# Performance work log

Hardware: AMD Instinct MI355X
Metric: run time of the kernel (lower is better)

The kernel has to match this reference:

```python
import jax, jax.numpy as jnp
import numpy as np

NX = 4096
NY = 4096
DX = 0.01
DY = 0.01
DT = 0.001
CX = 1.0
CY = 1.0
CXW = DT / DX / 2.0 * CX  # 0.05, x-direction stencil coefficient
CYW = DT / DY / 2.0 * CY  # 0.05, y-direction stencil coefficient
DIAG = 1.0                # A[1,1]
NLEVEL = int(np.log2(min(NX, NY))) + 1  # 13


def _smooth(x):
    # 3x3 cross-correlation with kernel A, valid padding (stride 1, no pad).
    # A[0,1]=CYW, A[2,1]=-CYW, A[1,0]=CXW, A[1,1]=1, A[1,2]=-CXW.
    return (CYW * x[:-2, 1:-1] - CYW * x[2:, 1:-1]
            + CXW * x[1:-1, :-2] + x[1:-1, 1:-1] - CXW * x[1:-1, 2:])


def _bc(u):
    # Replicate edges (not corners: corners stay exactly 0, as in the torch code).
    H, W = u.shape
    p = jnp.zeros((H + 2, W + 2), u.dtype)
    p = p.at[1:-1, 1:-1].set(u)
    p = p.at[0, 1:-1].set(u[0])
    p = p.at[-1, 1:-1].set(u[-1])
    p = p.at[1:-1, 0].set(u[:, 0])
    p = p.at[1:-1, -1].set(u[:, -1])
    return p


def _restrict(x):
    # 2x2 average pooling, stride 2 (conv weight = 0.25 everywhere).
    return 0.25 * (x[0::2, 0::2] + x[1::2, 0::2] + x[0::2, 1::2] + x[1::2, 1::2])


def _prolong(x):
    # Nearest-neighbor upsample by 2.
    return jnp.repeat(jnp.repeat(x, 2, axis=0), 2, axis=1)


def setup_inputs() -> dict:
    key = jax.random.key(0)
    u = jax.random.normal(key, (1, 1, NY, NX), dtype=jnp.float32)
    return {"u": u, "t": 4}


def reference(u, t):
    v = u[0, 0]  # (NY, NX)
    for _ in range(t):  # t outer F-cycle iterations (b = 0 source term)
        r = _smooth(_bc(v))  # residual on finest grid, (NY, NX)
        r_s = [r]
        for _i in range(1, NLEVEL - 3):
            r = _restrict(r)
            r_s.append(r)  # coarsest stored level is 8x8
        e = jnp.zeros((1, 1), v.dtype)
        for j in reversed(range(1, NLEVEL - 3)):
            # coarse-grid correction; broadcast of (small e) + r_s[j] matches torch
            e = e - _smooth(jnp.pad(e, 1)) / DIAG + r_s[j] / DIAG
            e = _prolong(e)
        v = v - e
        v = v - _smooth(_bc(v)) / DIAG
    return v[None, None]
```

## Files before the change

kernel.cpp:

```cpp
#include <hip/hip_runtime.h>
#include <cstddef>


constexpr float CW = 0.05f;

__device__ __forceinline__ float up_val(float Pc, float Pu, float Pd, float Pl,
                                        float Pr, float rv) {
  float sm = CW * Pu - CW * Pd + CW * Pl + Pc - CW * Pr;
  return (Pc - sm) + rv;
}

__global__ __launch_bounds__(256) void k_smooth_restrict(
    const float* __restrict__ v, float* __restrict__ r1) {
  const int n = 4096, h = 2048;
  int bj = blockIdx.x * blockDim.x + threadIdx.x;
  int bi = blockIdx.y * blockDim.y + threadIdx.y;
  int c0 = 4 * bj;
  int cl = max(c0 - 1, 0), cr = min(c0 + 4, n - 1);
  float a[6][6];
#pragma unroll
  for (int rr = 0; rr < 6; ++rr) {
    int R = min(max(4 * bi - 1 + rr, 0), n - 1);
    const float* row = v + (size_t)R * n;
    float4 m = *reinterpret_cast<const float4*>(row + c0);
    a[rr][0] = row[cl];
    a[rr][1] = m.x; a[rr][2] = m.y; a[rr][3] = m.z; a[rr][4] = m.w;
    a[rr][5] = row[cr];
  }
#pragma unroll
  for (int oi = 0; oi < 2; ++oi) {
    float2 o;
#pragma unroll
    for (int oj = 0; oj < 2; ++oj) {
      float s[2][2];
#pragma unroll
      for (int p = 0; p < 2; ++p)
#pragma unroll
        for (int q = 0; q < 2; ++q) {
          int P = 2 * oi + p, Q = 2 * oj + q;
          s[p][q] = CW * a[P][Q + 1] - CW * a[P + 2][Q + 1]
                  + CW * a[P + 1][Q] + a[P + 1][Q + 1] - CW * a[P + 1][Q + 2];
        }
      float val = 0.25f * (((s[0][0] + s[1][0]) + s[0][1]) + s[1][1]);
      (oj ? o.y : o.x) = val;
    }
    *reinterpret_cast<float2*>(r1 + (size_t)(2 * bi + oi) * h + 2 * bj) = o;
  }
}

__global__ __launch_bounds__(256) void k_restrict2(
    const float* __restrict__ x, float* __restrict__ y,
    float* __restrict__ z, int n) {
  int h = n >> 1, q = n >> 2;
  int j = blockIdx.x * blockDim.x + threadIdx.x;
  int i = blockIdx.y * blockDim.y + threadIdx.y;
  if (i >= q || 2 * j >= q) return;
  float xr[4][8];
#pragma unroll
  for (int rr = 0; rr < 4; ++rr) {
    const float* row = x + (size_t)(4 * i + rr) * n + 8 * j;
    float4 m0 = reinterpret_cast<const float4*>(row)[0];
    float4 m1 = reinterpret_cast<const float4*>(row)[1];
    xr[rr][0] = m0.x; xr[rr][1] = m0.y; xr[rr][2] = m0.z; xr[rr][3] = m0.w;
    xr[rr][4] = m1.x; xr[rr][5] = m1.y; xr[rr][6] = m1.z; xr[rr][7] = m1.w;
  }
  float yv[2][4];
#pragma unroll
  for (int a = 0; a < 2; ++a)
#pragma unroll
    for (int b = 0; b < 4; ++b)
      yv[a][b] = 0.25f * (((xr[2 * a][2 * b] + xr[2 * a + 1][2 * b])
                           + xr[2 * a][2 * b + 1]) + xr[2 * a + 1][2 * b + 1]);
#pragma unroll
  for (int a = 0; a < 2; ++a) {
    float4 o; o.x = yv[a][0]; o.y = yv[a][1]; o.z = yv[a][2]; o.w = yv[a][3];
    *reinterpret_cast<float4*>(y + (size_t)(2 * i + a) * h + 4 * j) = o;
  }
  float2 zo;
  zo.x = 0.25f * (((yv[0][0] + yv[1][0]) + yv[0][1]) + yv[1][1]);
  zo.y = 0.25f * (((yv[0][2] + yv[1][2]) + yv[0][3]) + yv[1][3]);
  *reinterpret_cast<float2*>(z + (size_t)i * q + 2 * j) = zo;
}

__global__ __launch_bounds__(256) void k_up(
    const float* __restrict__ Ep, const float* __restrict__ r,
    float* __restrict__ Eo, int n) {
  int s = n >> 1;
  int j = blockIdx.x * blockDim.x + threadIdx.x;
  int i = blockIdx.y * blockDim.y + threadIdx.y;
  if (i >= s || j >= (n >> 2)) return;
  const float* ec = Ep + (size_t)i * s + 2 * j;
  float epc0 = ec[0], epc1 = ec[1];
  float epl = (j > 0) ? ec[-1] : 0.0f;
  float epr = (2 * j + 2 < s) ? ec[2] : 0.0f;
  float epu0 = 0.0f, epu1 = 0.0f, epd0 = 0.0f, epd1 = 0.0f;
  if (i > 0)     { epu0 = ec[-s]; epu1 = ec[-s + 1]; }
  if (i < s - 1) { epd0 = ec[s];  epd1 = ec[s + 1]; }
  {
    float4 rv = *reinterpret_cast<const float4*>(r + (size_t)(2 * i) * n + 4 * j);
    float4 o;
    o.x = up_val(epc0, epu0, epc0, epl,  epc0, rv.x);
    o.y = up_val(epc0, epu0, epc0, epc0, epc1, rv.y);
    o.z = up_val(epc1, epu1, epc1, epc0, epc1, rv.z);
    o.w = up_val(epc1, epu1, epc1, epc1, epr,  rv.w);
    *reinterpret_cast<float4*>(Eo + (size_t)(2 * i) * n + 4 * j) = o;
  }
  {
    float4 rv = *reinterpret_cast<const float4*>(r + (size_t)(2 * i + 1) * n + 4 * j);
    float4 o;
    o.x = up_val(epc0, epc0, epd0, epl,  epc0, rv.x);
    o.y = up_val(epc0, epc0, epd0, epc0, epc1, rv.y);
    o.z = up_val(epc1, epc1, epd1, epc0, epc1, rv.z);
    o.w = up_val(epc1, epc1, epd1, epc1, epr,  rv.w);
    *reinterpret_cast<float4*>(Eo + (size_t)(2 * i + 1) * n + 4 * j) = o;
  }
}

__global__ void k_coarse(const float* __restrict__ r5, float* __restrict__ E5) {
  __shared__ float r6[64 * 64];
  __shared__ float r7[32 * 32];
  __shared__ float r8[16 * 16];
  __shared__ float r9[8 * 8];
  __shared__ float E8[16 * 16];
  __shared__ float E7[32 * 32];
  __shared__ float E6[64 * 64];
  int tid = threadIdx.x, nt = blockDim.x;

  auto up_lds = [&](const float* Ep, const float* rr, int i, int c, int nn) {
    int ss = nn >> 1;
    float Pc = Ep[(i >> 1) * ss + (c >> 1)];
    float Pu = (i > 0)      ? Ep[((i - 1) >> 1) * ss + (c >> 1)] : 0.0f;
    float Pd = (i < nn - 1) ? Ep[((i + 1) >> 1) * ss + (c >> 1)] : 0.0f;
    float Pl = (c > 0)      ? Ep[(i >> 1) * ss + ((c - 1) >> 1)] : 0.0f;
    float Pr = (c < nn - 1) ? Ep[(i >> 1) * ss + ((c + 1) >> 1)] : 0.0f;
    return up_val(Pc, Pu, Pd, Pl, Pr, rr[i * nn + c]);
  };

  for (int idx = tid; idx < 64 * 64; idx += nt) {
    int I = idx >> 6, J = idx & 63;
    float a = r5[(2 * I) * 128 + 2 * J],     b = r5[(2 * I + 1) * 128 + 2 * J];
    float c = r5[(2 * I) * 128 + 2 * J + 1], d = r5[(2 * I + 1) * 128 + 2 * J + 1];
    r6[idx] = 0.25f * (((a + b) + c) + d);
  }
  __syncthreads();
  for (int idx = tid; idx < 32 * 32; idx += nt) {
    int I = idx >> 5, J = idx & 31;
    float a = r6[(2 * I) * 64 + 2 * J],     b = r6[(2 * I + 1) * 64 + 2 * J];
    float c = r6[(2 * I) * 64 + 2 * J + 1], d = r6[(2 * I + 1) * 64 + 2 * J + 1];
    r7[idx] = 0.25f * (((a + b) + c) + d);
  }
  __syncthreads();
  for (int idx = tid; idx < 16 * 16; idx += nt) {
    int I = idx >> 4, J = idx & 15;
    float a = r7[(2 * I) * 32 + 2 * J],     b = r7[(2 * I + 1) * 32 + 2 * J];
    float c = r7[(2 * I) * 32 + 2 * J + 1], d = r7[(2 * I + 1) * 32 + 2 * J + 1];
    r8[idx] = 0.25f * (((a + b) + c) + d);
  }
  __syncthreads();
  for (int idx = tid; idx < 8 * 8; idx += nt) {
    int I = idx >> 3, J = idx & 7;
    float a = r8[(2 * I) * 16 + 2 * J],     b = r8[(2 * I + 1) * 16 + 2 * J];
    float c = r8[(2 * I) * 16 + 2 * J + 1], d = r8[(2 * I + 1) * 16 + 2 * J + 1];
    r9[idx] = 0.25f * (((a + b) + c) + d);
  }
  __syncthreads();
  for (int idx = tid; idx < 16 * 16; idx += nt)
    E8[idx] = up_lds(r9, r8, idx >> 4, idx & 15, 16);
  __syncthreads();
  for (int idx = tid; idx < 32 * 32; idx += nt)
    E7[idx] = up_lds(E8, r7, idx >> 5, idx & 31, 32);
  __syncthreads();
  for (int idx = tid; idx < 64 * 64; idx += nt)
    E6[idx] = up_lds(E7, r6, idx >> 6, idx & 63, 64);
  __syncthreads();
  for (int idx = tid; idx < 128 * 128; idx += nt)
    E5[idx] = up_lds(E6, r5, idx >> 7, idx & 127, 128);
}

__global__ __launch_bounds__(256) void k_final(
    const float* __restrict__ v, const float* __restrict__ E1,
    float* __restrict__ out) {
  const int n = 4096, h = 2048;
  int J = blockIdx.x * blockDim.x + threadIdx.x;
  int i = blockIdx.y * blockDim.y + threadIdx.y;
  int c0 = 4 * J;
  int cl = max(c0 - 1, 0), cr = min(c0 + 4, n - 1);
  int ecl = cl >> 1, ecr = cr >> 1;

  float e[3][4];
  int ers0 = max(2 * i - 1, 0) >> 1;
  int ers2 = min(2 * i + 2, n - 1) >> 1;
  const int ers[3] = {ers0, i, ers2};
#pragma unroll
  for (int t = 0; t < 3; ++t) {
    const float* erow = E1 + (size_t)ers[t] * h;
    e[t][0] = erow[ecl];
    e[t][1] = erow[2 * J];
    e[t][2] = erow[2 * J + 1];
    e[t][3] = erow[ecr];
  }

  float w[4][6];
  const int tmap[4] = {0, 1, 1, 2};
#pragma unroll
  for (int rr = 0; rr < 4; ++rr) {
    int R = min(max(2 * i - 1 + rr, 0), n - 1);
    int t = tmap[rr];
    const float* vrow = v + (size_t)R * n;
    float4 m = *reinterpret_cast<const float4*>(vrow + c0);
    w[rr][0] = vrow[cl] - e[t][0];
    w[rr][1] = m.x - e[t][1];
    w[rr][2] = m.y - e[t][1];
    w[rr][3] = m.z - e[t][2];
    w[rr][4] = m.w - e[t][2];
    w[rr][5] = vrow[cr] - e[t][3];
  }
#pragma unroll
  for (int a = 0; a < 2; ++a) {
    float4 o;
#pragma unroll
    for (int qq = 0; qq < 4; ++qq) {
      float ce = w[a + 1][qq + 1];
      float sm = CW * w[a][qq + 1] - CW * w[a + 2][qq + 1]
               + CW * w[a + 1][qq] + ce - CW * w[a + 1][qq + 2];
      (&o.x)[qq] = ce - sm;
    }
    *reinterpret_cast<float4*>(out + (size_t)(2 * i + a) * n + c0) = o;
  }
}

extern "C" void kernel_launch(void* const* d_in, const int* in_sizes, int n_in,
                              void* d_out, int out_size, void* d_ws, size_t ws_size,
                              hipStream_t stream) {
  (void)in_sizes; (void)n_in; (void)out_size;
  float* u = (float*)d_in[0];
  float* out = (float*)d_out;
  char* ws = (char*)d_ws;

  size_t off = 0;
  auto alloc = [&](size_t elems) {
    float* p = (float*)(ws + off);
    off += (elems * sizeof(float) + 255) & ~(size_t)255;
    return p;
  };
  float* r1 = alloc(2048 * 2048);
  float* r2 = alloc(1024 * 1024);
  float* r3 = alloc(512 * 512);
  float* r4 = alloc(256 * 256);
  float* r5 = alloc(128 * 128);
  float* E5 = alloc(128 * 128);
  float* E4 = alloc(256 * 256);
  float* E3 = alloc(512 * 512);
  float* E2 = alloc(1024 * 1024);
  float* E1 = alloc(2048 * 2048);
  size_t pool = off;
  const size_t VB = (size_t)4096 * 4096 * sizeof(float);
  bool big = ws_size >= pool + VB;
  float* vws = (float*)(ws + pool);

  dim3 b(64, 4);
  auto iterate = [&](const float* vin, float* vout) {
    k_smooth_restrict<<<dim3(16, 256), b, 0, stream>>>(vin, r1);
    k_restrict2<<<dim3(4, 128), b, 0, stream>>>(r1, r2, r3, 2048);
    k_restrict2<<<dim3(1, 32), b, 0, stream>>>(r3, r4, r5, 512);
    k_coarse<<<1, 1024, 0, stream>>>(r5, E5);
    k_up<<<dim3(1, 32), b, 0, stream>>>(E5, r4, E4, 256);
    k_up<<<dim3(2, 64), b, 0, stream>>>(E4, r3, E3, 512);
    k_up<<<dim3(4, 128), b, 0, stream>>>(E3, r2, E2, 1024);
    k_up<<<dim3(8, 256), b, 0, stream>>>(E2, r1, E1, 2048);
    k_final<<<dim3(16, 512), b, 0, stream>>>(vin, E1, vout);
  };

  if (big) {
    iterate(u, vws);
    iterate(vws, out);
    iterate(out, vws);
    iterate(vws, out);
  } else {
    iterate(u, out);
    iterate(out, u);
    iterate(u, out);
    iterate(out, u);
    hipMemcpyAsync(out, u, VB, hipMemcpyDeviceToDevice, stream);
  }
}
```

Before: 397.9 us.

## Fuse last prolongation, final smoothing and next-iteration residual restriction into one kernel

Replaces the finest k_up (building E1) and k_final with one tiled kernel. It computes the E1 tile in shared memory from E2 and r1, applies the correction and the post-smooth, writes v, and also computes the next iteration's smoothed-and-restricted residual from the new v. This drops the E1 round trip and the separate k_smooth_restrict pass in iterations 2-4, using double-buffered r1 storage. The cost is redundant halo computation, heavier shared-memory use per block (about 40 KB), and divisions and modulos in the index arithmetic.

```diff
diff --git a/kernel.cpp b/kernel.cpp
--- a/kernel.cpp
+++ b/kernel.cpp
@@ -177,55 +177,98 @@
     E5[idx] = up_lds(E6, r5, idx >> 7, idx & 127, 128);
 }
 
-__global__ __launch_bounds__(256) void k_final(
-    const float* __restrict__ v, const float* __restrict__ E1,
-    float* __restrict__ out) {
-  const int n = 4096, h = 2048;
-  int J = blockIdx.x * blockDim.x + threadIdx.x;
-  int i = blockIdx.y * blockDim.y + threadIdx.y;
-  int c0 = 4 * J;
-  int cl = max(c0 - 1, 0), cr = min(c0 + 4, n - 1);
-  int ecl = cl >> 1, ecr = cr >> 1;
-
-  float e[3][4];
-  int ers0 = max(2 * i - 1, 0) >> 1;
-  int ers2 = min(2 * i + 2, n - 1) >> 1;
-  const int ers[3] = {ers0, i, ers2};
-#pragma unroll
-  for (int t = 0; t < 3; ++t) {
-    const float* erow = E1 + (size_t)ers[t] * h;
-    e[t][0] = erow[ecl];
-    e[t][1] = erow[2 * J];
-    e[t][2] = erow[2 * J + 1];
-    e[t][3] = erow[ecr];
-  }
-
-  float w[4][6];
-  const int tmap[4] = {0, 1, 1, 2};
-#pragma unroll
-  for (int rr = 0; rr < 4; ++rr) {
-    int R = min(max(2 * i - 1 + rr, 0), n - 1);
-    int t = tmap[rr];
-    const float* vrow = v + (size_t)R * n;
-    float4 m = *reinterpret_cast<const float4*>(vrow + c0);
-    w[rr][0] = vrow[cl] - e[t][0];
-    w[rr][1] = m.x - e[t][1];
-    w[rr][2] = m.y - e[t][1];
-    w[rr][3] = m.z - e[t][2];
-    w[rr][4] = m.w - e[t][2];
-    w[rr][5] = vrow[cr] - e[t][3];
-  }
-#pragma unroll
-  for (int a = 0; a < 2; ++a) {
+template <bool WRITE_R1>
+__global__ __launch_bounds__(256) void k_fused(
+    const float* __restrict__ v, const float* __restrict__ E2,
+    const float* __restrict__ r1, float* __restrict__ vout,
+    float* __restrict__ r1o) {
+  const int n = 4096, h = 2048, s2 = 1024;
+  const int BI = 16, BJ = 256;
+  __shared__ float e1s[10][132];
+  __shared__ float wsh[20][264];
+  __shared__ float vps[18][264];
+  int tid = threadIdx.x;
+  int x0 = blockIdx.x * BJ;
+  int y0 = blockIdx.y * BI;
+  int eb_r = (y0 >> 1) - 1;
+  int eb_c = (x0 >> 1) - 1;
+
+  for (int idx = tid; idx < 10 * 130; idx += 256) {
+    int er = idx / 130, ec = idx % 130;
+    int gi = min(max(eb_r + er, 0), h - 1);
+    int gc = min(max(eb_c + ec, 0), h - 1);
+    float Pc = E2[(size_t)(gi >> 1) * s2 + (gc >> 1)];
+    float Pu = (gi > 0)     ? E2[(size_t)((gi - 1) >> 1) * s2 + (gc >> 1)] : 0.0f;
+    float Pd = (gi < h - 1) ? E2[(size_t)((gi + 1) >> 1) * s2 + (gc >> 1)] : 0.0f;
+    float Pl = (gc > 0)     ? E2[(size_t)(gi >> 1) * s2 + ((gc - 1) >> 1)] : 0.0f;
+    float Pr = (gc < h - 1) ? E2[(size_t)(gi >> 1) * s2 + ((gc + 1) >> 1)] : 0.0f;
+    e1s[er][ec] = up_val(Pc, Pu, Pd, Pl, Pr, r1[(size_t)gi * h + gc]);
+  }
+  __syncthreads();
+
+  for (int idx = tid; idx < 20 * 64; idx += 256) {
+    int wr = idx >> 6, f = idx & 63;
+    int Rc = min(max(y0 - 2 + wr, 0), n - 1);
+    int er = (Rc >> 1) - eb_r;
+    float4 m = *reinterpret_cast<const float4*>(v + (size_t)Rc * n + x0 + 4 * f);
+    float e0 = e1s[er][2 * f + 1], e1v = e1s[er][2 * f + 2];
+    wsh[wr][2 + 4 * f]     = m.x - e0;
+    wsh[wr][2 + 4 * f + 1] = m.y - e0;
+    wsh[wr][2 + 4 * f + 2] = m.z - e1v;
+    wsh[wr][2 + 4 * f + 3] = m.w - e1v;
+  }
+  for (int idx = tid; idx < 20 * 4; idx += 256) {
+    int wr = idx >> 2, k = idx & 3;
+    int wc = (k < 2) ? k : 256 + k;
+    int Rc = min(max(y0 - 2 + wr, 0), n - 1);
+    int Cc = min(max(x0 - 2 + wc, 0), n - 1);
+    int er = (Rc >> 1) - eb_r;
+    int ec = (Cc >> 1) - eb_c;
+    wsh[wr][wc] = v[(size_t)Rc * n + Cc] - e1s[er][ec];
+  }
+  __syncthreads();
+
+  for (int idx = tid; idx < 18 * 258; idx += 256) {
+    int pr = idx / 258, pc = idx % 258;
+    float wc = wsh[pr + 1][pc + 1];
+    float sm = CW * wsh[pr][pc + 1] - CW * wsh[pr + 2][pc + 1]
+             + CW * wsh[pr + 1][pc] + wc - CW * wsh[pr + 1][pc + 2];
+    vps[pr][pc] = wc - sm;
+  }
+  __syncthreads();
+
+  for (int idx = tid; idx < 16 * 64; idx += 256) {
+    int rr = idx >> 6, f = idx & 63;
     float4 o;
-#pragma unroll
-    for (int qq = 0; qq < 4; ++qq) {
-      float ce = w[a + 1][qq + 1];
-      float sm = CW * w[a][qq + 1] - CW * w[a + 2][qq + 1]
-               + CW * w[a + 1][qq] + ce - CW * w[a + 1][qq + 2];
-      (&o.x)[qq] = ce - sm;
+    o.x = vps[rr + 1][4 * f + 1];
+    o.y = vps[rr + 1][4 * f + 2];
+    o.z = vps[rr + 1][4 * f + 3];
+    o.w = vps[rr + 1][4 * f + 4];
+    *reinterpret_cast<float4*>(vout + (size_t)(y0 + rr) * n + x0 + 4 * f) = o;
+  }
+
+  if constexpr (WRITE_R1) {
+    for (int idx = tid; idx < 8 * 128; idx += 256) {
+      int a = idx >> 7, b = idx & 127;
+      int gi = (y0 >> 1) + a, gj = (x0 >> 1) + b;
+      float sacc[2][2];
+#pragma unroll
+      for (int p = 0; p < 2; ++p)
+#pragma unroll
+        for (int q = 0; q < 2; ++q) {
+          int R = 2 * gi + p, C = 2 * gj + q;
+          int Ru = max(R - 1, 0), Rd = min(R + 1, n - 1);
+          int Cl = max(C - 1, 0), Cr = min(C + 1, n - 1);
+          float ce = vps[R - y0 + 1][C - x0 + 1];
+          sacc[p][q] = CW * vps[Ru - y0 + 1][C - x0 + 1]
+                     - CW * vps[Rd - y0 + 1][C - x0 + 1]
+                     + CW * vps[R - y0 + 1][Cl - x0 + 1]
+                     + ce
+                     - CW * vps[R - y0 + 1][Cr - x0 + 1];
+        }
+      r1o[(size_t)gi * h + gj] =
+          0.25f * (((sacc[0][0] + sacc[1][0]) + sacc[0][1]) + sacc[1][1]);
     }
-    *reinterpret_cast<float4*>(out + (size_t)(2 * i + a) * n + c0) = o;
   }
 }
 
@@ -243,7 +286,8 @@
     off += (elems * sizeof(float) + 255) & ~(size_t)255;
     return p;
   };
-  float* r1 = alloc(2048 * 2048);
+  float* r1a = alloc(2048 * 2048);
+  float* r1b = alloc(2048 * 2048);
   float* r2 = alloc(1024 * 1024);
   float* r3 = alloc(512 * 512);
   float* r4 = alloc(256 * 256);
@@ -252,35 +296,41 @@
   float* E4 = alloc(256 * 256);
   float* E3 = alloc(512 * 512);
   float* E2 = alloc(1024 * 1024);
-  float* E1 = alloc(2048 * 2048);
   size_t pool = off;
   const size_t VB = (size_t)4096 * 4096 * sizeof(float);
   bool big = ws_size >= pool + VB;
   float* vws = (float*)(ws + pool);
 
   dim3 b(64, 4);
-  auto iterate = [&](const float* vin, float* vout) {
-    k_smooth_restrict<<<dim3(16, 256), b, 0, stream>>>(vin, r1);
+  auto pyramid = [&](const float* r1) {
     k_restrict2<<<dim3(4, 128), b, 0, stream>>>(r1, r2, r3, 2048);
     k_restrict2<<<dim3(1, 32), b, 0, stream>>>(r3, r4, r5, 512);
     k_coarse<<<1, 1024, 0, stream>>>(r5, E5);
     k_up<<<dim3(1, 32), b, 0, stream>>>(E5, r4, E4, 256);
     k_up<<<dim3(2, 64), b, 0, stream>>>(E4, r3, E3, 512);
     k_up<<<dim3(4, 128), b, 0, stream>>>(E3, r2, E2, 1024);
-    k_up<<<dim3(8, 256), b, 0, stream>>>(E2, r1, E1, 2048);
-    k_final<<<dim3(16, 512), b, 0, stream>>>(vin, E1, vout);
   };
-
+  dim3 fg(16, 256);
+
+  k_smooth_restrict<<<dim3(16, 256), b, 0, stream>>>(u, r1a);
   if (big) {
-    iterate(u, vws);
-    iterate(vws, out);
-    iterate(out, vws);
-    iterate(vws, out);
+    pyramid(r1a);
+    k_fused<true><<<fg, 256, 0, stream>>>(u, E2, r1a, vws, r1b);
+    pyramid(r1b);
+    k_fused<true><<<fg, 256, 0, stream>>>(vws, E2, r1b, out, r1a);
+    pyramid(r1a);
+    k_fused<true><<<fg, 256, 0, stream>>>(out, E2, r1a, vws, r1b);
+    pyramid(r1b);
+    k_fused<false><<<fg, 256, 0, stream>>>(vws, E2, r1b, out, nullptr);
   } else {
-    iterate(u, out);
-    iterate(out, u);
-    iterate(u, out);
-    iterate(out, u);
+    pyramid(r1a);
+    k_fused<true><<<fg, 256, 0, stream>>>(u, E2, r1a, out, r1b);
+    pyramid(r1b);
+    k_fused<true><<<fg, 256, 0, stream>>>(out, E2, r1b, u, r1a);
+    pyramid(r1a);
+    k_fused<true><<<fg, 256, 0, stream>>>(u, E2, r1a, out, r1b);
+    pyramid(r1b);
+    k_fused<false><<<fg, 256, 0, stream>>>(out, E2, r1b, u, nullptr);
     hipMemcpyAsync(out, u, VB, hipMemcpyDeviceToDevice, stream);
   }
 }
```

Measured after the change: 516.4 us. +29.8%, slower.

## Fuse restriction pyramid, coarse solve and prolongation into one persistent kernel with grid barriers

Applied to the files above, without the earlier changes.

Replaces the seven launches per iteration (two restrict kernels, the single-block coarse solve and four prolongation kernels) with one persistent 128-block kernel. Stages are separated by atomic-counter grid barriers, and a counter reset kernel runs once at the start. Every block recomputes the coarse levels 6-9 in LDS and produces only its own two rows of E4, so the serial single-block coarse stage disappears. This removes launch gaps and small-grid tail latency, but the big prolongation stages now run on only 128 blocks of 256 threads, which may underuse the GPU's bandwidth, and correctness relies on all 128 blocks being co-resident.

```diff
diff --git a/kernel.cpp b/kernel.cpp
--- a/kernel.cpp
+++ b/kernel.cpp
@@ -3,11 +3,30 @@
 
 
 constexpr float CW = 0.05f;
+#define NBLK 128u
 
 __device__ __forceinline__ float up_val(float Pc, float Pu, float Pd, float Pl,
                                         float Pr, float rv) {
   float sm = CW * Pu - CW * Pd + CW * Pl + Pc - CW * Pr;
   return (Pc - sm) + rv;
+}
+
+__device__ __forceinline__ void grid_barrier(unsigned int* cnt, unsigned int target) {
+  __syncthreads();
+  __threadfence();
+  if (threadIdx.x == 0) {
+    __hip_atomic_fetch_add(cnt, 1u, __ATOMIC_ACQ_REL, __HIP_MEMORY_SCOPE_AGENT);
+    while (__hip_atomic_load(cnt, __ATOMIC_RELAXED, __HIP_MEMORY_SCOPE_AGENT) < target) {
+      __builtin_amdgcn_s_sleep(1);
+    }
+  }
+  __syncthreads();
+  __threadfence();
+}
+
+__global__ void k_zero(unsigned int* p, int n) {
+  int i = blockIdx.x * blockDim.x + threadIdx.x;
+  if (i < n) p[i] = 0u;
 }
 
 __global__ __launch_bounds__(256) void k_smooth_restrict(
@@ -48,47 +67,11 @@
   }
 }
 
-__global__ __launch_bounds__(256) void k_restrict2(
-    const float* __restrict__ x, float* __restrict__ y,
-    float* __restrict__ z, int n) {
-  int h = n >> 1, q = n >> 2;
-  int j = blockIdx.x * blockDim.x + threadIdx.x;
-  int i = blockIdx.y * blockDim.y + threadIdx.y;
-  if (i >= q || 2 * j >= q) return;
-  float xr[4][8];
-#pragma unroll
-  for (int rr = 0; rr < 4; ++rr) {
-    const float* row = x + (size_t)(4 * i + rr) * n + 8 * j;
-    float4 m0 = reinterpret_cast<const float4*>(row)[0];
-    float4 m1 = reinterpret_cast<const float4*>(row)[1];
-    xr[rr][0] = m0.x; xr[rr][1] = m0.y; xr[rr][2] = m0.z; xr[rr][3] = m0.w;
-    xr[rr][4] = m1.x; xr[rr][5] = m1.y; xr[rr][6] = m1.z; xr[rr][7] = m1.w;
-  }
-  float yv[2][4];
-#pragma unroll
-  for (int a = 0; a < 2; ++a)
-#pragma unroll
-    for (int b = 0; b < 4; ++b)
-      yv[a][b] = 0.25f * (((xr[2 * a][2 * b] + xr[2 * a + 1][2 * b])
-                           + xr[2 * a][2 * b + 1]) + xr[2 * a + 1][2 * b + 1]);
-#pragma unroll
-  for (int a = 0; a < 2; ++a) {
-    float4 o; o.x = yv[a][0]; o.y = yv[a][1]; o.z = yv[a][2]; o.w = yv[a][3];
-    *reinterpret_cast<float4*>(y + (size_t)(2 * i + a) * h + 4 * j) = o;
-  }
-  float2 zo;
-  zo.x = 0.25f * (((yv[0][0] + yv[1][0]) + yv[0][1]) + yv[1][1]);
-  zo.y = 0.25f * (((yv[0][2] + yv[1][2]) + yv[0][3]) + yv[1][3]);
-  *reinterpret_cast<float2*>(z + (size_t)i * q + 2 * j) = zo;
-}
-
-__global__ __launch_bounds__(256) void k_up(
-    const float* __restrict__ Ep, const float* __restrict__ r,
-    float* __restrict__ Eo, int n) {
+__device__ __forceinline__ void up_tile24(const float* __restrict__ Ep,
+                                          const float* __restrict__ r,
+                                          float* __restrict__ Eo,
+                                          int n, int i, int j) {
   int s = n >> 1;
-  int j = blockIdx.x * blockDim.x + threadIdx.x;
-  int i = blockIdx.y * blockDim.y + threadIdx.y;
-  if (i >= s || j >= (n >> 2)) return;
   const float* ec = Ep + (size_t)i * s + 2 * j;
   float epc0 = ec[0], epc1 = ec[1];
   float epl = (j > 0) ? ec[-1] : 0.0f;
@@ -116,65 +99,162 @@
   }
 }
 
-__global__ void k_coarse(const float* __restrict__ r5, float* __restrict__ E5) {
-  __shared__ float r6[64 * 64];
-  __shared__ float r7[32 * 32];
-  __shared__ float r8[16 * 16];
-  __shared__ float r9[8 * 8];
-  __shared__ float E8[16 * 16];
-  __shared__ float E7[32 * 32];
-  __shared__ float E6[64 * 64];
-  int tid = threadIdx.x, nt = blockDim.x;
-
-  auto up_lds = [&](const float* Ep, const float* rr, int i, int c, int nn) {
-    int ss = nn >> 1;
-    float Pc = Ep[(i >> 1) * ss + (c >> 1)];
-    float Pu = (i > 0)      ? Ep[((i - 1) >> 1) * ss + (c >> 1)] : 0.0f;
-    float Pd = (i < nn - 1) ? Ep[((i + 1) >> 1) * ss + (c >> 1)] : 0.0f;
-    float Pl = (c > 0)      ? Ep[(i >> 1) * ss + ((c - 1) >> 1)] : 0.0f;
-    float Pr = (c < nn - 1) ? Ep[(i >> 1) * ss + ((c + 1) >> 1)] : 0.0f;
-    return up_val(Pc, Pu, Pd, Pl, Pr, rr[i * nn + c]);
-  };
-
-  for (int idx = tid; idx < 64 * 64; idx += nt) {
-    int I = idx >> 6, J = idx & 63;
-    float a = r5[(2 * I) * 128 + 2 * J],     b = r5[(2 * I + 1) * 128 + 2 * J];
-    float c = r5[(2 * I) * 128 + 2 * J + 1], d = r5[(2 * I + 1) * 128 + 2 * J + 1];
-    r6[idx] = 0.25f * (((a + b) + c) + d);
-  }
-  __syncthreads();
-  for (int idx = tid; idx < 32 * 32; idx += nt) {
-    int I = idx >> 5, J = idx & 31;
-    float a = r6[(2 * I) * 64 + 2 * J],     b = r6[(2 * I + 1) * 64 + 2 * J];
-    float c = r6[(2 * I) * 64 + 2 * J + 1], d = r6[(2 * I + 1) * 64 + 2 * J + 1];
-    r7[idx] = 0.25f * (((a + b) + c) + d);
-  }
-  __syncthreads();
-  for (int idx = tid; idx < 16 * 16; idx += nt) {
-    int I = idx >> 4, J = idx & 15;
-    float a = r7[(2 * I) * 32 + 2 * J],     b = r7[(2 * I + 1) * 32 + 2 * J];
-    float c = r7[(2 * I) * 32 + 2 * J + 1], d = r7[(2 * I + 1) * 32 + 2 * J + 1];
-    r8[idx] = 0.25f * (((a + b) + c) + d);
-  }
-  __syncthreads();
-  for (int idx = tid; idx < 8 * 8; idx += nt) {
-    int I = idx >> 3, J = idx & 7;
-    float a = r8[(2 * I) * 16 + 2 * J],     b = r8[(2 * I + 1) * 16 + 2 * J];
-    float c = r8[(2 * I) * 16 + 2 * J + 1], d = r8[(2 * I + 1) * 16 + 2 * J + 1];
-    r9[idx] = 0.25f * (((a + b) + c) + d);
-  }
-  __syncthreads();
-  for (int idx = tid; idx < 16 * 16; idx += nt)
-    E8[idx] = up_lds(r9, r8, idx >> 4, idx & 15, 16);
-  __syncthreads();
-  for (int idx = tid; idx < 32 * 32; idx += nt)
-    E7[idx] = up_lds(E8, r7, idx >> 5, idx & 31, 32);
-  __syncthreads();
-  for (int idx = tid; idx < 64 * 64; idx += nt)
-    E6[idx] = up_lds(E7, r6, idx >> 6, idx & 63, 64);
-  __syncthreads();
-  for (int idx = tid; idx < 128 * 128; idx += nt)
-    E5[idx] = up_lds(E6, r5, idx >> 7, idx & 127, 128);
+__global__ __launch_bounds__(256, 1) void k_pyramid(
+    const float* __restrict__ r1, float* __restrict__ r2,
+    float* __restrict__ r3, float* __restrict__ r4, float* __restrict__ r5,
+    float* __restrict__ E4, float* __restrict__ E3, float* __restrict__ E2,
+    float* __restrict__ E1, unsigned int* __restrict__ bars) {
+  __shared__ float r5s[128 * 128];
+  __shared__ float r6s[64 * 64];
+  __shared__ float r7s[32 * 32];
+  __shared__ float r8s[16 * 16];
+  __shared__ float r9s[8 * 8];
+  __shared__ float E8s[16 * 16];
+  __shared__ float E7s[32 * 32];
+  __shared__ float E6s[64 * 64];
+  __shared__ float e5r[3][128];
+  int tid = threadIdx.x;
+  int bid = blockIdx.x;
+  int g = bid * 256 + tid;
+
+  if (g < 16384) {
+    int i5 = g >> 7, j5 = g & 127;
+    const float* src = r1 + (size_t)(i5 << 4) * 2048 + (j5 << 4);
+    float rr2[8][8];
+#pragma unroll
+    for (int a = 0; a < 8; ++a) {
+      float ta[16], tb[16];
+      const float* ra = src + (size_t)(2 * a) * 2048;
+      const float* rb = ra + 2048;
+#pragma unroll
+      for (int q = 0; q < 4; ++q) {
+        *reinterpret_cast<float4*>(ta + 4 * q) = reinterpret_cast<const float4*>(ra)[q];
+        *reinterpret_cast<float4*>(tb + 4 * q) = reinterpret_cast<const float4*>(rb)[q];
+      }
+#pragma unroll
+      for (int b = 0; b < 8; ++b)
+        rr2[a][b] = 0.25f * (((ta[2 * b] + tb[2 * b]) + ta[2 * b + 1]) + tb[2 * b + 1]);
+      float* dst = r2 + (size_t)((i5 << 3) + a) * 1024 + (j5 << 3);
+      float4 o0, o1;
+      o0.x = rr2[a][0]; o0.y = rr2[a][1]; o0.z = rr2[a][2]; o0.w = rr2[a][3];
+      o1.x = rr2[a][4]; o1.y = rr2[a][5]; o1.z = rr2[a][6]; o1.w = rr2[a][7];
+      reinterpret_cast<float4*>(dst)[0] = o0;
+      reinterpret_cast<float4*>(dst)[1] = o1;
+    }
+    float rr3[4][4];
+#pragma unroll
+    for (int a = 0; a < 4; ++a) {
+#pragma unroll
+      for (int b = 0; b < 4; ++b)
+        rr3[a][b] = 0.25f * (((rr2[2 * a][2 * b] + rr2[2 * a + 1][2 * b])
+                              + rr2[2 * a][2 * b + 1]) + rr2[2 * a + 1][2 * b + 1]);
+      float4 o;
+      o.x = rr3[a][0]; o.y = rr3[a][1]; o.z = rr3[a][2]; o.w = rr3[a][3];
+      *reinterpret_cast<float4*>(r3 + (size_t)((i5 << 2) + a) * 512 + (j5 << 2)) = o;
+    }
+    float rr4[2][2];
+#pragma unroll
+    for (int a = 0; a < 2; ++a) {
+#pragma unroll
+      for (int b = 0; b < 2; ++b)
+        rr4[a][b] = 0.25f * (((rr3[2 * a][2 * b] + rr3[2 * a + 1][2 * b])
+                              + rr3[2 * a][2 * b + 1]) + rr3[2 * a + 1][2 * b + 1]);
+      float2 o;
+      o.x = rr4[a][0]; o.y = rr4[a][1];
+      *reinterpret_cast<float2*>(r4 + (size_t)((i5 << 1) + a) * 256 + (j5 << 1)) = o;
+    }
+    r5[(size_t)i5 * 128 + j5] =
+        0.25f * (((rr4[0][0] + rr4[1][0]) + rr4[0][1]) + rr4[1][1]);
+  }
+  grid_barrier(bars + 0, NBLK);
+
+  {
+    auto up_lds = [&](const float* Ep, const float* rr, int i, int c, int nn) {
+      int ss = nn >> 1;
+      float Pc = Ep[(i >> 1) * ss + (c >> 1)];
+      float Pu = (i > 0)      ? Ep[((i - 1) >> 1) * ss + (c >> 1)] : 0.0f;
+      float Pd = (i < nn - 1) ? Ep[((i + 1) >> 1) * ss + (c >> 1)] : 0.0f;
+      float Pl = (c > 0)      ? Ep[(i >> 1) * ss + ((c - 1) >> 1)] : 0.0f;
+      float Pr = (c < nn - 1) ? Ep[(i >> 1) * ss + ((c + 1) >> 1)] : 0.0f;
+      return up_val(Pc, Pu, Pd, Pl, Pr, rr[i * nn + c]);
+    };
+    for (int idx = tid; idx < 4096; idx += 256)
+      reinterpret_cast<float4*>(r5s)[idx] = reinterpret_cast<const float4*>(r5)[idx];
+    __syncthreads();
+    for (int idx = tid; idx < 64 * 64; idx += 256) {
+      int I = idx >> 6, J = idx & 63;
+      float a = r5s[(2 * I) * 128 + 2 * J],     b = r5s[(2 * I + 1) * 128 + 2 * J];
+      float c = r5s[(2 * I) * 128 + 2 * J + 1], d = r5s[(2 * I + 1) * 128 + 2 * J + 1];
+      r6s[idx] = 0.25f * (((a + b) + c) + d);
+    }
+    __syncthreads();
+    for (int idx = tid; idx < 32 * 32; idx += 256) {
+      int I = idx >> 5, J = idx & 31;
+      float a = r6s[(2 * I) * 64 + 2 * J],     b = r6s[(2 * I + 1) * 64 + 2 * J];
+      float c = r6s[(2 * I) * 64 + 2 * J + 1], d = r6s[(2 * I + 1) * 64 + 2 * J + 1];
+      r7s[idx] = 0.25f * (((a + b) + c) + d);
+    }
+    __syncthreads();
+    for (int idx = tid; idx < 16 * 16; idx += 256) {
+      int I = idx >> 4, J = idx & 15;
+      float a = r7s[(2 * I) * 32 + 2 * J],     b = r7s[(2 * I + 1) * 32 + 2 * J];
+      float c = r7s[(2 * I) * 32 + 2 * J + 1], d = r7s[(2 * I + 1) * 32 + 2 * J + 1];
+      r8s[idx] = 0.25f * (((a + b) + c) + d);
+    }
+    __syncthreads();
+    for (int idx = tid; idx < 8 * 8; idx += 256) {
+      int I = idx >> 3, J = idx & 7;
+      float a = r8s[(2 * I) * 16 + 2 * J],     b = r8s[(2 * I + 1) * 16 + 2 * J];
+      float c = r8s[(2 * I) * 16 + 2 * J + 1], d = r8s[(2 * I + 1) * 16 + 2 * J + 1];
+      r9s[idx] = 0.25f * (((a + b) + c) + d);
+    }
+    __syncthreads();
+    for (int idx = tid; idx < 16 * 16; idx += 256)
+      E8s[idx] = up_lds(r9s, r8s, idx >> 4, idx & 15, 16);
+    __syncthreads();
+    for (int idx = tid; idx < 32 * 32; idx += 256)
+      E7s[idx] = up_lds(E8s, r7s, idx >> 5, idx & 31, 32);
+    __syncthreads();
+    for (int idx = tid; idx < 64 * 64; idx += 256)
+      E6s[idx] = up_lds(E7s, r6s, idx >> 6, idx & 63, 64);
+    __syncthreads();
+    for (int idx = tid; idx < 3 * 128; idx += 256) {
+      int rr = idx >> 7, c = idx & 127;
+      int i = min(max(bid - 1 + rr, 0), 127);
+      e5r[rr][c] = up_lds(E6s, r5s, i, c, 128);
+    }
+    __syncthreads();
+    for (int idx = tid; idx < 512; idx += 256) {
+      int gi = 2 * bid + (idx >> 8);
+      int gc = idx & 255;
+      float Pc = e5r[1][gc >> 1];
+      float Pu = (gi > 0)   ? e5r[((gi - 1) >> 1) - bid + 1][gc >> 1] : 0.0f;
+      float Pd = (gi < 255) ? e5r[((gi + 1) >> 1) - bid + 1][gc >> 1] : 0.0f;
+      float Pl = (gc > 0)   ? e5r[1][(gc - 1) >> 1] : 0.0f;
+      float Pr = (gc < 255) ? e5r[1][(gc + 1) >> 1] : 0.0f;
+      E4[(size_t)gi * 256 + gc] = up_val(Pc, Pu, Pd, Pl, Pr, r4[(size_t)gi * 256 + gc]);
+    }
+  }
+  grid_barrier(bars + 1, NBLK);
+
+  {
+    int i = g >> 7, j = g & 127;
+    up_tile24(E4, r3, E3, 512, i, j);
+  }
+  grid_barrier(bars + 2, NBLK);
+
+#pragma unroll
+  for (int t = 0; t < 4; ++t) {
+    int tile = g + t * 32768;
+    up_tile24(E3, r2, E2, 1024, tile >> 8, tile & 255);
+  }
+  grid_barrier(bars + 3, NBLK);
+
+#pragma unroll
+  for (int t = 0; t < 16; ++t) {
+    int tile = g + t * 32768;
+    up_tile24(E2, r1, E1, 2048, tile >> 9, tile & 511);
+  }
 }
 
 __global__ __launch_bounds__(256) void k_final(
@@ -248,39 +328,35 @@
   float* r3 = alloc(512 * 512);
   float* r4 = alloc(256 * 256);
   float* r5 = alloc(128 * 128);
-  float* E5 = alloc(128 * 128);
   float* E4 = alloc(256 * 256);
   float* E3 = alloc(512 * 512);
   float* E2 = alloc(1024 * 1024);
   float* E1 = alloc(2048 * 2048);
+  unsigned int* bars = (unsigned int*)alloc(64);
   size_t pool = off;
   const size_t VB = (size_t)4096 * 4096 * sizeof(float);
   bool big = ws_size >= pool + VB;
   float* vws = (float*)(ws + pool);
 
   dim3 b(64, 4);
-  auto iterate = [&](const float* vin, float* vout) {
+  auto iterate = [&](const float* vin, float* vout, int it) {
     k_smooth_restrict<<<dim3(16, 256), b, 0, stream>>>(vin, r1);
-    k_restrict2<<<dim3(4, 128), b, 0, stream>>>(r1, r2, r3, 2048);
-    k_restrict2<<<dim3(1, 32), b, 0, stream>>>(r3, r4, r5, 512);
-    k_coarse<<<1, 1024, 0, stream>>>(r5, E5);
-    k_up<<<dim3(1, 32), b, 0, stream>>>(E5, r4, E4, 256);
-    k_up<<<dim3(2, 64), b, 0, stream>>>(E4, r3, E3, 512);
-    k_up<<<dim3(4, 128), b, 0, stream>>>(E3, r2, E2, 1024);
-    k_up<<<dim3(8, 256), b, 0, stream>>>(E2, r1, E1, 2048);
+    k_pyramid<<<NBLK, 256, 0, stream>>>(r1, r2, r3, r4, r5, E4, E3, E2, E1,
+                                        bars + 4 * it);
     k_final<<<dim3(16, 512), b, 0, stream>>>(vin, E1, vout);
   };
 
+  k_zero<<<1, 64, 0, stream>>>(bars, 16);
   if (big) {
-    iterate(u, vws);
-    iterate(vws, out);
-    iterate(out, vws);
-    iterate(vws, out);
+    iterate(u, vws, 0);
+    iterate(vws, out, 1);
+    iterate(out, vws, 2);
+    iterate(vws, out, 3);
   } else {
-    iterate(u, out);
-    iterate(out, u);
-    iterate(u, out);
-    iterate(out, u);
+    iterate(u, out, 0);
+    iterate(out, u, 1);
+    iterate(u, out, 2);
+    iterate(out, u, 3);
     hipMemcpyAsync(out, u, VB, hipMemcpyDeviceToDevice, stream);
   }
 }
```

Measured after the change: 808.5 us. +103.2%, slower.

## Fuse restriction chain and coarse/upsample levels into fewer kernels

Applied to the files above, without the earlier changes.

Merges the fine smooth-restrict and all restriction levels down to 128x128 into one tiled kernel that keeps intermediates in shared memory. The coarse solve is extended to produce E4 directly, with the block count raised from 1 to 16; each block recomputes the full coarse pyramid redundantly. Two upsample levels (E3 and E2) are fused with E3 held in LDS. This cuts the launch count per iteration from 9 to 5 and removes some intermediate global round trips, at the cost of redundant coarse work and lower occupancy in the chain kernel.

```diff
diff --git a/kernel.cpp b/kernel.cpp
--- a/kernel.cpp
+++ b/kernel.cpp
@@ -10,76 +10,228 @@
   return (Pc - sm) + rv;
 }
 
-__global__ __launch_bounds__(256) void k_smooth_restrict(
-    const float* __restrict__ v, float* __restrict__ r1) {
+__global__ __launch_bounds__(256) void k_sr_chain(
+    const float* __restrict__ v, float* __restrict__ r1,
+    float* __restrict__ r2, float* __restrict__ r3,
+    float* __restrict__ r4, float* __restrict__ r5) {
   const int n = 4096, h = 2048;
-  int bj = blockIdx.x * blockDim.x + threadIdx.x;
-  int bi = blockIdx.y * blockDim.y + threadIdx.y;
-  int c0 = 4 * bj;
-  int cl = max(c0 - 1, 0), cr = min(c0 + 4, n - 1);
-  float a[6][6];
-#pragma unroll
-  for (int rr = 0; rr < 6; ++rr) {
-    int R = min(max(4 * bi - 1 + rr, 0), n - 1);
-    const float* row = v + (size_t)R * n;
-    float4 m = *reinterpret_cast<const float4*>(row + c0);
-    a[rr][0] = row[cl];
-    a[rr][1] = m.x; a[rr][2] = m.y; a[rr][3] = m.z; a[rr][4] = m.w;
-    a[rr][5] = row[cr];
-  }
-#pragma unroll
-  for (int oi = 0; oi < 2; ++oi) {
-    float2 o;
-#pragma unroll
-    for (int oj = 0; oj < 2; ++oj) {
-      float s[2][2];
-#pragma unroll
-      for (int p = 0; p < 2; ++p)
-#pragma unroll
-        for (int q = 0; q < 2; ++q) {
-          int P = 2 * oi + p, Q = 2 * oj + q;
-          s[p][q] = CW * a[P][Q + 1] - CW * a[P + 2][Q + 1]
-                  + CW * a[P + 1][Q] + a[P + 1][Q + 1] - CW * a[P + 1][Q + 2];
-        }
-      float val = 0.25f * (((s[0][0] + s[1][0]) + s[0][1]) + s[1][1]);
-      (oj ? o.y : o.x) = val;
-    }
-    *reinterpret_cast<float2*>(r1 + (size_t)(2 * bi + oi) * h + 2 * bj) = o;
-  }
-}
-
-__global__ __launch_bounds__(256) void k_restrict2(
-    const float* __restrict__ x, float* __restrict__ y,
-    float* __restrict__ z, int n) {
-  int h = n >> 1, q = n >> 2;
-  int j = blockIdx.x * blockDim.x + threadIdx.x;
-  int i = blockIdx.y * blockDim.y + threadIdx.y;
-  if (i >= q || 2 * j >= q) return;
-  float xr[4][8];
-#pragma unroll
-  for (int rr = 0; rr < 4; ++rr) {
-    const float* row = x + (size_t)(4 * i + rr) * n + 8 * j;
-    float4 m0 = reinterpret_cast<const float4*>(row)[0];
-    float4 m1 = reinterpret_cast<const float4*>(row)[1];
-    xr[rr][0] = m0.x; xr[rr][1] = m0.y; xr[rr][2] = m0.z; xr[rr][3] = m0.w;
-    xr[rr][4] = m1.x; xr[rr][5] = m1.y; xr[rr][6] = m1.z; xr[rr][7] = m1.w;
-  }
-  float yv[2][4];
-#pragma unroll
-  for (int a = 0; a < 2; ++a)
-#pragma unroll
-    for (int b = 0; b < 4; ++b)
-      yv[a][b] = 0.25f * (((xr[2 * a][2 * b] + xr[2 * a + 1][2 * b])
-                           + xr[2 * a][2 * b + 1]) + xr[2 * a + 1][2 * b + 1]);
-#pragma unroll
-  for (int a = 0; a < 2; ++a) {
-    float4 o; o.x = yv[a][0]; o.y = yv[a][1]; o.z = yv[a][2]; o.w = yv[a][3];
-    *reinterpret_cast<float4*>(y + (size_t)(2 * i + a) * h + 4 * j) = o;
-  }
-  float2 zo;
-  zo.x = 0.25f * (((yv[0][0] + yv[1][0]) + yv[0][1]) + yv[1][1]);
-  zo.y = 0.25f * (((yv[0][2] + yv[1][2]) + yv[0][3]) + yv[1][3]);
-  *reinterpret_cast<float2*>(z + (size_t)i * q + 2 * j) = zo;
+  __shared__ float r1s[64][65];
+  __shared__ float r2s[32][33];
+  __shared__ float r3s[16][17];
+  __shared__ float r4s[8][9];
+  int tid = threadIdx.x;
+  int bx = blockIdx.x, by = blockIdx.y;
+  int ty0 = by * 64, tx0 = bx * 64;
+
+#pragma unroll
+  for (int k = 0; k < 4; ++k) {
+    int u = tid + 256 * k;
+    int uy = u >> 5, ux = u & 31;
+    int bi = (ty0 >> 1) + uy;
+    int bj = (tx0 >> 1) + ux;
+    int c0 = 4 * bj;
+    int cl = max(c0 - 1, 0), cr = min(c0 + 4, n - 1);
+    float a[6][6];
+#pragma unroll
+    for (int rr = 0; rr < 6; ++rr) {
+      int R = min(max(4 * bi - 1 + rr, 0), n - 1);
+      const float* row = v + (size_t)R * n;
+      float4 m = *reinterpret_cast<const float4*>(row + c0);
+      a[rr][0] = row[cl];
+      a[rr][1] = m.x; a[rr][2] = m.y; a[rr][3] = m.z; a[rr][4] = m.w;
+      a[rr][5] = row[cr];
+    }
+#pragma unroll
+    for (int oi = 0; oi < 2; ++oi) {
+      float2 o;
+#pragma unroll
+      for (int oj = 0; oj < 2; ++oj) {
+        float s[2][2];
+#pragma unroll
+        for (int p = 0; p < 2; ++p)
+#pragma unroll
+          for (int q = 0; q < 2; ++q) {
+            int P = 2 * oi + p, Q = 2 * oj + q;
+            s[p][q] = CW * a[P][Q + 1] - CW * a[P + 2][Q + 1]
+                    + CW * a[P + 1][Q] + a[P + 1][Q + 1] - CW * a[P + 1][Q + 2];
+          }
+        float val = 0.25f * (((s[0][0] + s[1][0]) + s[0][1]) + s[1][1]);
+        (oj ? o.y : o.x) = val;
+        r1s[2 * uy + oi][2 * ux + oj] = val;
+      }
+      *reinterpret_cast<float2*>(r1 + (size_t)(2 * bi + oi) * h + 2 * bj) = o;
+    }
+  }
+  __syncthreads();
+
+#pragma unroll
+  for (int k = 0; k < 4; ++k) {
+    int idx = tid + 256 * k;
+    int I = idx >> 5, J = idx & 31;
+    float val = 0.25f * (((r1s[2 * I][2 * J] + r1s[2 * I + 1][2 * J])
+                          + r1s[2 * I][2 * J + 1]) + r1s[2 * I + 1][2 * J + 1]);
+    r2s[I][J] = val;
+    r2[(size_t)(32 * by + I) * 1024 + 32 * bx + J] = val;
+  }
+  __syncthreads();
+
+  {
+    int I = tid >> 4, J = tid & 15;
+    float val = 0.25f * (((r2s[2 * I][2 * J] + r2s[2 * I + 1][2 * J])
+                          + r2s[2 * I][2 * J + 1]) + r2s[2 * I + 1][2 * J + 1]);
+    r3s[I][J] = val;
+    r3[(size_t)(16 * by + I) * 512 + 16 * bx + J] = val;
+  }
+  __syncthreads();
+
+  if (tid < 64) {
+    int I = tid >> 3, J = tid & 7;
+    float val = 0.25f * (((r3s[2 * I][2 * J] + r3s[2 * I + 1][2 * J])
+                          + r3s[2 * I][2 * J + 1]) + r3s[2 * I + 1][2 * J + 1]);
+    r4s[I][J] = val;
+    r4[(size_t)(8 * by + I) * 256 + 8 * bx + J] = val;
+  }
+  __syncthreads();
+
+  if (tid < 16) {
+    int I = tid >> 2, J = tid & 3;
+    float val = 0.25f * (((r4s[2 * I][2 * J] + r4s[2 * I + 1][2 * J])
+                          + r4s[2 * I][2 * J + 1]) + r4s[2 * I + 1][2 * J + 1]);
+    r5[(size_t)(4 * by + I) * 128 + 4 * bx + J] = val;
+  }
+}
+
+__global__ __launch_bounds__(1024, 1) void k_coarse_ext(
+    const float* __restrict__ r5, const float* __restrict__ r4,
+    float* __restrict__ E4) {
+  __shared__ float r5s[128 * 128];
+  __shared__ float r6s[64 * 64];
+  __shared__ float r7s[32 * 32];
+  __shared__ float r8s[16 * 16];
+  __shared__ float r9s[8 * 8];
+  __shared__ float E8s[16 * 16];
+  __shared__ float E7s[32 * 32];
+  __shared__ float E6s[64 * 64];
+  __shared__ float e5r[10][128];
+  int tid = threadIdx.x;
+  int bid = blockIdx.x;
+
+  auto up_lds = [&](const float* Ep, const float* rr, int i, int c, int nn) {
+    int ss = nn >> 1;
+    float Pc = Ep[(i >> 1) * ss + (c >> 1)];
+    float Pu = (i > 0)      ? Ep[((i - 1) >> 1) * ss + (c >> 1)] : 0.0f;
+    float Pd = (i < nn - 1) ? Ep[((i + 1) >> 1) * ss + (c >> 1)] : 0.0f;
+    float Pl = (c > 0)      ? Ep[(i >> 1) * ss + ((c - 1) >> 1)] : 0.0f;
+    float Pr = (c < nn - 1) ? Ep[(i >> 1) * ss + ((c + 1) >> 1)] : 0.0f;
+    return up_val(Pc, Pu, Pd, Pl, Pr, rr[i * nn + c]);
+  };
+
+  for (int idx = tid; idx < 4096; idx += 1024)
+    reinterpret_cast<float4*>(r5s)[idx] = reinterpret_cast<const float4*>(r5)[idx];
+  __syncthreads();
+  for (int idx = tid; idx < 64 * 64; idx += 1024) {
+    int I = idx >> 6, J = idx & 63;
+    float a = r5s[(2 * I) * 128 + 2 * J],     b = r5s[(2 * I + 1) * 128 + 2 * J];
+    float c = r5s[(2 * I) * 128 + 2 * J + 1], d = r5s[(2 * I + 1) * 128 + 2 * J + 1];
+    r6s[idx] = 0.25f * (((a + b) + c) + d);
+  }
+  __syncthreads();
+  if (tid < 32 * 32) {
+    int I = tid >> 5, J = tid & 31;
+    float a = r6s[(2 * I) * 64 + 2 * J],     b = r6s[(2 * I + 1) * 64 + 2 * J];
+    float c = r6s[(2 * I) * 64 + 2 * J + 1], d = r6s[(2 * I + 1) * 64 + 2 * J + 1];
+    r7s[tid] = 0.25f * (((a + b) + c) + d);
+  }
+  __syncthreads();
+  if (tid < 16 * 16) {
+    int I = tid >> 4, J = tid & 15;
+    float a = r7s[(2 * I) * 32 + 2 * J],     b = r7s[(2 * I + 1) * 32 + 2 * J];
+    float c = r7s[(2 * I) * 32 + 2 * J + 1], d = r7s[(2 * I + 1) * 32 + 2 * J + 1];
+    r8s[tid] = 0.25f * (((a + b) + c) + d);
+  }
+  __syncthreads();
+  if (tid < 8 * 8) {
+    int I = tid >> 3, J = tid & 7;
+    float a = r8s[(2 * I) * 16 + 2 * J],     b = r8s[(2 * I + 1) * 16 + 2 * J];
+    float c = r8s[(2 * I) * 16 + 2 * J + 1], d = r8s[(2 * I + 1) * 16 + 2 * J + 1];
+    r9s[tid] = 0.25f * (((a + b) + c) + d);
+  }
+  __syncthreads();
+  if (tid < 16 * 16)
+    E8s[tid] = up_lds(r9s, r8s, tid >> 4, tid & 15, 16);
+  __syncthreads();
+  if (tid < 32 * 32)
+    E7s[tid] = up_lds(E8s, r7s, tid >> 5, tid & 31, 32);
+  __syncthreads();
+  for (int idx = tid; idx < 64 * 64; idx += 1024)
+    E6s[idx] = up_lds(E7s, r6s, idx >> 6, idx & 63, 64);
+  __syncthreads();
+  for (int idx = tid; idx < 10 * 128; idx += 1024) {
+    int t = idx >> 7, c = idx & 127;
+    int i = min(max(8 * bid - 1 + t, 0), 127);
+    e5r[t][c] = up_lds(E6s, r5s, i, c, 128);
+  }
+  __syncthreads();
+  for (int idx = tid; idx < 16 * 256; idx += 1024) {
+    int gi = 16 * bid + (idx >> 8);
+    int gc = idx & 255;
+    float Pc = e5r[(gi >> 1) - 8 * bid + 1][gc >> 1];
+    float Pu = (gi > 0)   ? e5r[((gi - 1) >> 1) - 8 * bid + 1][gc >> 1] : 0.0f;
+    float Pd = (gi < 255) ? e5r[((gi + 1) >> 1) - 8 * bid + 1][gc >> 1] : 0.0f;
+    float Pl = (gc > 0)   ? e5r[(gi >> 1) - 8 * bid + 1][(gc - 1) >> 1] : 0.0f;
+    float Pr = (gc < 255) ? e5r[(gi >> 1) - 8 * bid + 1][(gc + 1) >> 1] : 0.0f;
+    E4[(size_t)gi * 256 + gc] = up_val(Pc, Pu, Pd, Pl, Pr, r4[(size_t)gi * 256 + gc]);
+  }
+}
+
+__global__ __launch_bounds__(256) void k_up_e3e2(
+    const float* __restrict__ E4, const float* __restrict__ r3,
+    const float* __restrict__ r2, float* __restrict__ E2) {
+  __shared__ float e3s[34][35];
+  int tid = threadIdx.x;
+  int bx = blockIdx.x, by = blockIdx.y;
+  int br0 = 32 * by - 1, bc0 = 32 * bx - 1;
+
+  for (int idx = tid; idx < 34 * 34; idx += 256) {
+    int er = idx / 34, ec = idx % 34;
+    int gr = br0 + er, gc = bc0 + ec;
+    float val = 0.0f;
+    if (gr >= 0 && gr < 512 && gc >= 0 && gc < 512) {
+      float Pc = E4[(size_t)(gr >> 1) * 256 + (gc >> 1)];
+      float Pu = (gr > 0)   ? E4[(size_t)((gr - 1) >> 1) * 256 + (gc >> 1)] : 0.0f;
+      float Pd = (gr < 511) ? E4[(size_t)((gr + 1) >> 1) * 256 + (gc >> 1)] : 0.0f;
+      float Pl = (gc > 0)   ? E4[(size_t)(gr >> 1) * 256 + ((gc - 1) >> 1)] : 0.0f;
+      float Pr = (gc < 511) ? E4[(size_t)(gr >> 1) * 256 + ((gc + 1) >> 1)] : 0.0f;
+      val = up_val(Pc, Pu, Pd, Pl, Pr, r3[(size_t)gr * 512 + gc]);
+    }
+    e3s[er][ec] = val;
+  }
+  __syncthreads();
+
+#pragma unroll
+  for (int k = 0; k < 4; ++k) {
+    int u = tid + 256 * k;
+    int rr = u >> 4, f = u & 15;
+    int gR = 64 * by + rr;
+    int gC = 64 * bx + 4 * f;
+    int rc = (gR >> 1) - br0;
+    int ru = ((gR - 1) >> 1) - br0;
+    int rd = ((gR + 1) >> 1) - br0;
+    float4 rv = *reinterpret_cast<const float4*>(r2 + (size_t)gR * 1024 + gC);
+    float4 o;
+#pragma unroll
+    for (int q = 0; q < 4; ++q) {
+      int c = gC + q;
+      int lc = (c >> 1) - bc0;
+      float Pc = e3s[rc][lc];
+      float Pu = (gR > 0)    ? e3s[ru][lc] : 0.0f;
+      float Pd = (gR < 1023) ? e3s[rd][lc] : 0.0f;
+      float Pl = (c > 0)     ? e3s[rc][((c - 1) >> 1) - bc0] : 0.0f;
+      float Pr = (c < 1023)  ? e3s[rc][((c + 1) >> 1) - bc0] : 0.0f;
+      (&o.x)[q] = up_val(Pc, Pu, Pd, Pl, Pr, (&rv.x)[q]);
+    }
+    *reinterpret_cast<float4*>(E2 + (size_t)gR * 1024 + gC) = o;
+  }
 }
 
 __global__ __launch_bounds__(256) void k_up(
@@ -116,67 +268,6 @@
   }
 }
 
-__global__ void k_coarse(const float* __restrict__ r5, float* __restrict__ E5) {
-  __shared__ float r6[64 * 64];
-  __shared__ float r7[32 * 32];
-  __shared__ float r8[16 * 16];
-  __shared__ float r9[8 * 8];
-  __shared__ float E8[16 * 16];
-  __shared__ float E7[32 * 32];
-  __shared__ float E6[64 * 64];
-  int tid = threadIdx.x, nt = blockDim.x;
-
-  auto up_lds = [&](const float* Ep, const float* rr, int i, int c, int nn) {
-    int ss = nn >> 1;
-    float Pc = Ep[(i >> 1) * ss + (c >> 1)];
-    float Pu = (i > 0)      ? Ep[((i - 1) >> 1) * ss + (c >> 1)] : 0.0f;
-    float Pd = (i < nn - 1) ? Ep[((i + 1) >> 1) * ss + (c >> 1)] : 0.0f;
-    float Pl = (c > 0)      ? Ep[(i >> 1) * ss + ((c - 1) >> 1)] : 0.0f;
-    float Pr = (c < nn - 1) ? Ep[(i >> 1) * ss + ((c + 1) >> 1)] : 0.0f;
-    return up_val(Pc, Pu, Pd, Pl, Pr, rr[i * nn + c]);
-  };
-
-  for (int idx = tid; idx < 64 * 64; idx += nt) {
-    int I = idx >> 6, J = idx & 63;
-    float a = r5[(2 * I) * 128 + 2 * J],     b = r5[(2 * I + 1) * 128 + 2 * J];
-    float c = r5[(2 * I) * 128 + 2 * J + 1], d = r5[(2 * I + 1) * 128 + 2 * J + 1];
-    r6[idx] = 0.25f * (((a + b) + c) + d);
-  }
-  __syncthreads();
-  for (int idx = tid; idx < 32 * 32; idx += nt) {
-    int I = idx >> 5, J = idx & 31;
-    float a = r6[(2 * I) * 64 + 2 * J],     b = r6[(2 * I + 1) * 64 + 2 * J];
-    float c = r6[(2 * I) * 64 + 2 * J + 1], d = r6[(2 * I + 1) * 64 + 2 * J + 1];
-    r7[idx] = 0.25f * (((a + b) + c) + d);
-  }
-  __syncthreads();
-  for (int idx = tid; idx < 16 * 16; idx += nt) {
-    int I = idx >> 4, J = idx & 15;
-    float a = r7[(2 * I) * 32 + 2 * J],     b = r7[(2 * I + 1) * 32 + 2 * J];
-    float c = r7[(2 * I) * 32 + 2 * J + 1], d = r7[(2 * I + 1) * 32 + 2 * J + 1];
-    r8[idx] = 0.25f * (((a + b) + c) + d);
-  }
-  __syncthreads();
-  for (int idx = tid; idx < 8 * 8; idx += nt) {
-    int I = idx >> 3, J = idx & 7;
-    float a = r8[(2 * I) * 16 + 2 * J],     b = r8[(2 * I + 1) * 16 + 2 * J];
-    float c = r8[(2 * I) * 16 + 2 * J + 1], d = r8[(2 * I + 1) * 16 + 2 * J + 1];
-    r9[idx] = 0.25f * (((a + b) + c) + d);
-  }
-  __syncthreads();
-  for (int idx = tid; idx < 16 * 16; idx += nt)
-    E8[idx] = up_lds(r9, r8, idx >> 4, idx & 15, 16);
-  __syncthreads();
-  for (int idx = tid; idx < 32 * 32; idx += nt)
-    E7[idx] = up_lds(E8, r7, idx >> 5, idx & 31, 32);
-  __syncthreads();
-  for (int idx = tid; idx < 64 * 64; idx += nt)
-    E6[idx] = up_lds(E7, r6, idx >> 6, idx & 63, 64);
-  __syncthreads();
-  for (int idx = tid; idx < 128 * 128; idx += nt)
-    E5[idx] = up_lds(E6, r5, idx >> 7, idx & 127, 128);
-}
-
 __global__ __launch_bounds__(256) void k_final(
     const float* __restrict__ v, const float* __restrict__ E1,
     float* __restrict__ out) {
@@ -248,9 +339,7 @@
   float* r3 = alloc(512 * 512);
   float* r4 = alloc(256 * 256);
   float* r5 = alloc(128 * 128);
-  float* E5 = alloc(128 * 128);
   float* E4 = alloc(256 * 256);
-  float* E3 = alloc(512 * 512);
   float* E2 = alloc(1024 * 1024);
   float* E1 = alloc(2048 * 2048);
   size_t pool = off;
@@ -260,13 +349,9 @@
 
   dim3 b(64, 4);
   auto iterate = [&](const float* vin, float* vout) {
-    k_smooth_restrict<<<dim3(16, 256), b, 0, stream>>>(vin, r1);
-    k_restrict2<<<dim3(4, 128), b, 0, stream>>>(r1, r2, r3, 2048);
-    k_restrict2<<<dim3(1, 32), b, 0, stream>>>(r3, r4, r5, 512);
-    k_coarse<<<1, 1024, 0, stream>>>(r5, E5);
-    k_up<<<dim3(1, 32), b, 0, stream>>>(E5, r4, E4, 256);
-    k_up<<<dim3(2, 64), b, 0, stream>>>(E4, r3, E3, 512);
-    k_up<<<dim3(4, 128), b, 0, stream>>>(E3, r2, E2, 1024);
+    k_sr_chain<<<dim3(32, 32), 256, 0, stream>>>(vin, r1, r2, r3, r4, r5);
+    k_coarse_ext<<<16, 1024, 0, stream>>>(r5, r4, E4);
+    k_up_e3e2<<<dim3(16, 16), 256, 0, stream>>>(E4, r3, r2, E2);
     k_up<<<dim3(8, 256), b, 0, stream>>>(E2, r1, E1, 2048);
     k_final<<<dim3(16, 512), b, 0, stream>>>(vin, E1, vout);
   };
```

Measured after the change: 380.4 us. -4.4%, faster.
